# Performance work log

Measured on AMD Instinct MI355X. Metric: run time of the kernel, lower is better.

Reference implementation:

```python
import jax, jax.numpy as jnp
import numpy as np

B, N, R = 16, 512, 10
DE, DR, DOUT = 256, 64, 256

def setup_inputs() -> dict:
    key = jax.random.key(0)
    k1, k2, k3, k4 = jax.random.split(key, 4)
    node_features = jax.random.normal(k1, (B, N, DE), dtype=jnp.float32)
    relation_features = jax.random.normal(k2, (B, R, DR), dtype=jnp.float32)
    adj = jax.random.uniform(k3, (B, R, N, N), dtype=jnp.float32)
    in_dim = (DE + DR) * R
    bound = float(np.sqrt(6.0 / (in_dim + DOUT)))  # xavier_uniform
    W = jax.random.uniform(k4, (DOUT, in_dim), dtype=jnp.float32, minval=-bound, maxval=bound)
    bias = jnp.zeros((DOUT,), dtype=jnp.float32)
    return {"node_features": node_features, "relation_features": relation_features,
            "adj": adj, "W": W, "bias": bias}

def reference(node_features, relation_features, adj, W, bias):
    # adj: [B,R,N,N]; node_features: [B,N,De]; relation_features: [B,R,Dr]
    # Per relation r: bmm(adj[:,r], cat([node, rel_r broadcast], -1))
    # Node part: adj @ node_features for every relation at once.
    node_part = jnp.einsum('brnm,bmd->brnd', adj, node_features)      # [B,R,N,De]
    # Relation part: adj @ (rel_r repeated over rows) == rowsum(adj) * rel_r
    rel_part = adj.sum(axis=-1)[..., None] * relation_features[:, :, None, :]  # [B,R,N,Dr]
    supports = jnp.concatenate([node_part, rel_part], axis=-1)        # [B,R,N,De+Dr]
    supports = supports.transpose(0, 2, 1, 3).reshape(node_features.shape[0],
                                                      node_features.shape[1], -1)  # [B,N,R*(De+Dr)]
    return supports @ W.T + bias
```

## Files before the change

kernel.cpp:

```cpp
#include <hip/hip_runtime.h>
#include <stdint.h>

#define B_     16
#define N_     512
#define R_     10
#define DE_    256
#define DR_    64
#define DOUT_  256
#define INDIM_ 3200
#define BLK_   320
#define RN_    5120
#define SPLITS_ 5

typedef __bf16          v8bf  __attribute__((ext_vector_type(8)));
typedef unsigned short  v8us  __attribute__((ext_vector_type(8)));
typedef float           f32x4 __attribute__((ext_vector_type(4)));

static __device__ __forceinline__ unsigned short f2b(float f) {
  union { float f; unsigned u; } c; c.f = f;
  unsigned r = c.u + 0x7FFFu + ((c.u >> 16) & 1u);
  return (unsigned short)(r >> 16);
}

static __device__ __forceinline__ v8bf us2bf(v8us u) {
  union { v8us u; v8bf b; } c; c.u = u; return c.b;
}

static __device__ __forceinline__ void gl_lds16(const void* g, void* l) {
  __builtin_amdgcn_global_load_lds(
      (const __attribute__((address_space(1))) void*)g,
      (__attribute__((address_space(3))) void*)l, 16, 0, 0);
}

__global__ void prep_nodeB(const float* __restrict__ nf, unsigned short* __restrict__ nodeB) {
  const size_t base = (size_t)blockIdx.x * 8192;
  const int tid = threadIdx.x;
#pragma unroll
  for (int p = 0; p < 4; ++p) {
    size_t off = base + (size_t)p * 2048 + (size_t)tid * 8;
    float4 x = *(const float4*)(nf + off);
    float4 y = *(const float4*)(nf + off + 4);
    v8us u;
    u[0] = f2b(x.x); u[1] = f2b(x.y); u[2] = f2b(x.z); u[3] = f2b(x.w);
    u[4] = f2b(y.x); u[5] = f2b(y.y); u[6] = f2b(y.z); u[7] = f2b(y.w);
    *(v8us*)(nodeB + off) = u;
  }
}

__global__ void prep_W(const float* __restrict__ W, unsigned short* __restrict__ Wn) {
  int idx = blockIdx.x * 256 + threadIdx.x;
  int r = idx >> 16;
  int o = (idx >> 8) & 255;
  int d = idx & 255;
  Wn[idx] = f2b(W[(size_t)o * INDIM_ + r * BLK_ + d]);
}

__global__ void prep_U(const float* __restrict__ rel, const float* __restrict__ W,
                       float* __restrict__ Uf) {
  int idx = blockIdx.x * 256 + threadIdx.x;
  int o  = idx & 255;
  int br = idx >> 8;
  int r  = br % R_;
  const float* rp = rel + (size_t)br * DR_;
  const float* wp = W + (size_t)o * INDIM_ + r * BLK_ + DE_;
  float v = 0.f;
#pragma unroll 8
  for (int d = 0; d < DR_; ++d) v += rp[d] * wp[d];
  Uf[idx] = v;
}

__global__ void stageA_gemm(const unsigned short* __restrict__ nodeB,
                            const unsigned short* __restrict__ WnB,
                            const float* __restrict__ Uf,
                            unsigned short* __restrict__ Gp) {
  __shared__ unsigned short Al[128 * 64];
  __shared__ unsigned short Bl[128 * 64];
  const int br = blockIdx.x;
  const int b  = br / R_, r = br % R_;
  const int o0 = blockIdx.y * 128;
  const int m0 = blockIdx.z * 128;
  const int tid  = threadIdx.x;
  const int lane = tid & 63;
  const int wave = tid >> 6;
  const int wm = wave >> 1, wn = wave & 1;
  const int quad = lane >> 4, l16 = lane & 15;

  const unsigned short* Wb = WnB + (size_t)r * (DOUT_ * DE_);
  const unsigned short* Nb = nodeB + (size_t)b * (N_ * DE_);

  f32x4 acc[4][4];
#pragma unroll
  for (int i = 0; i < 4; ++i)
#pragma unroll
    for (int j = 0; j < 4; ++j) acc[i][j] = f32x4{0.f, 0.f, 0.f, 0.f};

  for (int dk = 0; dk < DE_; dk += 64) {
#pragma unroll
    for (int it = 0; it < 4; ++it) {
      int rowblk = it * 32 + wave * 8;
      int rl = rowblk + (lane >> 3);
      int kc = (lane & 7) ^ (rl & 7);
      gl_lds16(Wb + (size_t)(o0 + rl) * DE_ + dk + kc * 8, Al + rowblk * 64);
      gl_lds16(Nb + (size_t)(m0 + rl) * DE_ + dk + kc * 8, Bl + rowblk * 64);
    }
    __syncthreads();
#pragma unroll
    for (int ks = 0; ks < 2; ++ks) {
      const int kb = ks * 4;
      v8bf av[4], bv[4];
#pragma unroll
      for (int mi = 0; mi < 4; ++mi) {
        int m = wm * 64 + mi * 16 + l16;
        av[mi] = us2bf(*(const v8us*)(Al + m * 64 + (((kb + quad) ^ (m & 7)) * 8)));
      }
#pragma unroll
      for (int ni = 0; ni < 4; ++ni) {
        int c = wn * 64 + ni * 16 + l16;
        bv[ni] = us2bf(*(const v8us*)(Bl + c * 64 + (((kb + quad) ^ (c & 7)) * 8)));
      }
#pragma unroll
      for (int mi = 0; mi < 4; ++mi)
#pragma unroll
        for (int ni = 0; ni < 4; ++ni)
          acc[mi][ni] = __builtin_amdgcn_mfma_f32_16x16x32_bf16(av[mi], bv[ni], acc[mi][ni], 0, 0, 0);
    }
    __syncthreads();
  }

#pragma unroll
  for (int mi = 0; mi < 4; ++mi)
#pragma unroll
    for (int t = 0; t < 4; ++t) {
      int o = o0 + wm * 64 + mi * 16 + quad * 4 + t;
      float u = Uf[(size_t)br * DOUT_ + o];
      unsigned short* grow = Gp + ((size_t)(b * DOUT_ + o)) * RN_ + r * N_ + m0;
#pragma unroll
      for (int ni = 0; ni < 4; ++ni) {
        int m = wn * 64 + ni * 16 + l16;
        grow[m] = f2b(acc[mi][ni][t] + u);
      }
    }
}

__global__ __launch_bounds__(256, 3)
void stageB_gemm(const float* __restrict__ adj,
                 const unsigned short* __restrict__ Gp,
                 float* __restrict__ part) {
  __shared__ unsigned short Al[64 * 64];
  __shared__ unsigned short Bl[256 * 64];
  const int b  = blockIdx.x;
  const int n0 = blockIdx.y * 64;
  const int sp = blockIdx.z;
  const int tid  = threadIdx.x;
  const int lane = tid & 63;
  const int wave = tid >> 6;
  const int quad = lane >> 4, l16 = lane & 15;

  const float* Ab = adj + (size_t)b * (R_ * N_ * N_);
  const unsigned short* Gb = Gp + (size_t)b * (DOUT_ * RN_);

  f32x4 acc[4][4];
#pragma unroll
  for (int i = 0; i < 4; ++i)
#pragma unroll
    for (int j = 0; j < 4; ++j) acc[i][j] = f32x4{0.f, 0.f, 0.f, 0.f};

  const int arow = tid >> 2;
  const int acb  = tid & 3;
  const float* arp = Ab + (size_t)(n0 + arow) * N_ + acb * 16;

  float4 p0, p1, p2, p3;
  {
    const float* g = arp + (size_t)(sp * 2) * (N_ * N_);
    p0 = *(const float4*)(g);
    p1 = *(const float4*)(g + 4);
    p2 = *(const float4*)(g + 8);
    p3 = *(const float4*)(g + 12);
  }

  for (int it = 0; it < 16; ++it) {
    const int r  = sp * 2 + (it >> 3);
    const int k0 = r * N_ + (it & 7) * 64;
#pragma unroll
    for (int s = 0; s < 8; ++s) {
      int rowblk = s * 32 + wave * 8;
      int rl = rowblk + (lane >> 3);
      int kc = (lane & 7) ^ (rl & 7);
      gl_lds16(Gb + (size_t)rl * RN_ + k0 + kc * 8, Bl + rowblk * 64);
    }
    {
      v8us u0, u1;
      u0[0] = f2b(p0.x); u0[1] = f2b(p0.y); u0[2] = f2b(p0.z); u0[3] = f2b(p0.w);
      u0[4] = f2b(p1.x); u0[5] = f2b(p1.y); u0[6] = f2b(p1.z); u0[7] = f2b(p1.w);
      u1[0] = f2b(p2.x); u1[1] = f2b(p2.y); u1[2] = f2b(p2.z); u1[3] = f2b(p2.w);
      u1[4] = f2b(p3.x); u1[5] = f2b(p3.y); u1[6] = f2b(p3.z); u1[7] = f2b(p3.w);
      int c0 = (acb * 2)     ^ (arow & 7);
      int c1 = (acb * 2 + 1) ^ (arow & 7);
      *(v8us*)(Al + arow * 64 + c0 * 8) = u0;
      *(v8us*)(Al + arow * 64 + c1 * 8) = u1;
    }
    if (it < 15) {
      const int rn = sp * 2 + ((it + 1) >> 3);
      const float* g = arp + (size_t)rn * (N_ * N_) + ((it + 1) & 7) * 64;
      p0 = *(const float4*)(g);
      p1 = *(const float4*)(g + 4);
      p2 = *(const float4*)(g + 8);
      p3 = *(const float4*)(g + 12);
    }
    __syncthreads();
#pragma unroll
    for (int ks = 0; ks < 2; ++ks) {
      const int kb = ks * 4;
      v8bf av[4], bv[4];
#pragma unroll
      for (int mi = 0; mi < 4; ++mi) {
        int m = mi * 16 + l16;
        av[mi] = us2bf(*(const v8us*)(Al + m * 64 + (((kb + quad) ^ (m & 7)) * 8)));
      }
#pragma unroll
      for (int ni = 0; ni < 4; ++ni) {
        int o = wave * 64 + ni * 16 + l16;
        bv[ni] = us2bf(*(const v8us*)(Bl + o * 64 + (((kb + quad) ^ (o & 7)) * 8)));
      }
#pragma unroll
      for (int mi = 0; mi < 4; ++mi)
#pragma unroll
        for (int ni = 0; ni < 4; ++ni)
          acc[mi][ni] = __builtin_amdgcn_mfma_f32_16x16x32_bf16(av[mi], bv[ni], acc[mi][ni], 0, 0, 0);
    }
    __syncthreads();
  }

  float* pb = part + (((size_t)sp * B_ + b) * N_) * DOUT_;
#pragma unroll
  for (int mi = 0; mi < 4; ++mi)
#pragma unroll
    for (int t = 0; t < 4; ++t) {
      int row = n0 + mi * 16 + quad * 4 + t;
#pragma unroll
      for (int ni = 0; ni < 4; ++ni) {
        int col = wave * 64 + ni * 16 + l16;
        pb[(size_t)row * DOUT_ + col] = acc[mi][ni][t];
      }
    }
}

__global__ void reduce_out(const float* __restrict__ part, const float* __restrict__ bias,
                           float* __restrict__ out) {
  const size_t idx = (size_t)blockIdx.x * 256 + threadIdx.x;
  const size_t stride = (size_t)B_ * N_ * DOUT_ / 4;
  f32x4 a = *(const f32x4*)(bias + (idx & 63) * 4);
#pragma unroll
  for (int s = 0; s < SPLITS_; ++s) {
    f32x4 p = *(const f32x4*)((const float*)part + (stride * s + idx) * 4);
    a += p;
  }
  *(f32x4*)(out + idx * 4) = a;
}

extern "C" void kernel_launch(void* const* d_in, const int* in_sizes, int n_in,
                              void* d_out, int out_size, void* d_ws, size_t ws_size,
                              hipStream_t stream) {
  const float* node = (const float*)d_in[0];
  const float* rel  = (const float*)d_in[1];
  const float* adj  = (const float*)d_in[2];
  const float* W    = (const float*)d_in[3];
  const float* bias = (const float*)d_in[4];
  float* out = (float*)d_out;

  char* ws = (char*)d_ws;
  unsigned short* nodeB = (unsigned short*)(ws);
  unsigned short* WnB   = (unsigned short*)(ws + ((size_t)5 << 20));
  float*          Uf    = (float*)         (ws + ((size_t)7 << 20));
  unsigned short* Gp    = (unsigned short*)(ws + ((size_t)8 << 20));
  float*          part  = (float*)         (ws + ((size_t)48 << 20));

  prep_nodeB<<<dim3((B_ * N_ * DE_) / 8192), 256, 0, stream>>>(node, nodeB);
  prep_W<<<dim3((R_ * DOUT_ * DE_) / 256), 256, 0, stream>>>(W, WnB);
  prep_U<<<dim3((B_ * R_ * DOUT_) / 256), 256, 0, stream>>>(rel, W, Uf);
  stageA_gemm<<<dim3(B_ * R_, DOUT_ / 128, N_ / 128), 256, 0, stream>>>(nodeB, WnB, Uf, Gp);
  stageB_gemm<<<dim3(B_, N_ / 64, SPLITS_), 256, 0, stream>>>(adj, Gp, part);
  reduce_out<<<dim3((B_ * N_ * DOUT_ / 4) / 256), 256, 0, stream>>>(part, bias, out);
}
```

Before: 321.9 us.

## Merge prep kernels, stage Gp stores through LDS, shrink stageB row tile

The three preprocessing kernels become a single launch that branches on block index, and the W conversion is vectorized to four elements per thread. stageA now writes its bf16 output tile into shared memory and then stores it to Gp with coalesced 16-byte writes, replacing scattered 2-byte stores. stageB halves its row tile from 64 to 32, which doubles the grid and raises launch_bounds occupancy to 4 blocks per CU. The smaller tile means each block re-reads the full 256-column Gp tile for half as many rows, doubling Gp traffic from L2 in exchange for more parallelism.

Measured after the change: 314.9 us. -2.2%, faster.

```diff
diff --git a/kernel.cpp b/kernel.cpp
--- a/kernel.cpp
+++ b/kernel.cpp
@@ -14,6 +14,7 @@
 
 typedef __bf16          v8bf  __attribute__((ext_vector_type(8)));
 typedef unsigned short  v8us  __attribute__((ext_vector_type(8)));
+typedef unsigned short  v4us  __attribute__((ext_vector_type(4)));
 typedef float           f32x4 __attribute__((ext_vector_type(4)));
 
 static __device__ __forceinline__ unsigned short f2b(float f) {
@@ -32,49 +33,55 @@
       (__attribute__((address_space(3))) void*)l, 16, 0, 0);
 }
 
-__global__ void prep_nodeB(const float* __restrict__ nf, unsigned short* __restrict__ nodeB) {
-  const size_t base = (size_t)blockIdx.x * 8192;
+__global__ void prep_all(const float* __restrict__ nf, const float* __restrict__ W,
+                         const float* __restrict__ rel,
+                         unsigned short* __restrict__ nodeB,
+                         unsigned short* __restrict__ WnB,
+                         float* __restrict__ Uf) {
+  const int bb = blockIdx.x;
   const int tid = threadIdx.x;
-#pragma unroll
-  for (int p = 0; p < 4; ++p) {
-    size_t off = base + (size_t)p * 2048 + (size_t)tid * 8;
-    float4 x = *(const float4*)(nf + off);
-    float4 y = *(const float4*)(nf + off + 4);
-    v8us u;
+  if (bb < 256) {
+    const size_t base = (size_t)bb * 8192;
+#pragma unroll
+    for (int p = 0; p < 4; ++p) {
+      size_t off = base + (size_t)p * 2048 + (size_t)tid * 8;
+      float4 x = *(const float4*)(nf + off);
+      float4 y = *(const float4*)(nf + off + 4);
+      v8us u;
+      u[0] = f2b(x.x); u[1] = f2b(x.y); u[2] = f2b(x.z); u[3] = f2b(x.w);
+      u[4] = f2b(y.x); u[5] = f2b(y.y); u[6] = f2b(y.z); u[7] = f2b(y.w);
+      *(v8us*)(nodeB + off) = u;
+    }
+  } else if (bb < 896) {
+    int idx = (bb - 256) * 1024 + tid * 4;
+    int r = idx >> 16;
+    int o = (idx >> 8) & 255;
+    int d = idx & 255;
+    float4 x = *(const float4*)(W + (size_t)o * INDIM_ + r * BLK_ + d);
+    v4us u;
     u[0] = f2b(x.x); u[1] = f2b(x.y); u[2] = f2b(x.z); u[3] = f2b(x.w);
-    u[4] = f2b(y.x); u[5] = f2b(y.y); u[6] = f2b(y.z); u[7] = f2b(y.w);
-    *(v8us*)(nodeB + off) = u;
-  }
-}
-
-__global__ void prep_W(const float* __restrict__ W, unsigned short* __restrict__ Wn) {
-  int idx = blockIdx.x * 256 + threadIdx.x;
-  int r = idx >> 16;
-  int o = (idx >> 8) & 255;
-  int d = idx & 255;
-  Wn[idx] = f2b(W[(size_t)o * INDIM_ + r * BLK_ + d]);
-}
-
-__global__ void prep_U(const float* __restrict__ rel, const float* __restrict__ W,
-                       float* __restrict__ Uf) {
-  int idx = blockIdx.x * 256 + threadIdx.x;
-  int o  = idx & 255;
-  int br = idx >> 8;
-  int r  = br % R_;
-  const float* rp = rel + (size_t)br * DR_;
-  const float* wp = W + (size_t)o * INDIM_ + r * BLK_ + DE_;
-  float v = 0.f;
+    *(v4us*)(WnB + idx) = u;
+  } else {
+    int idx = (bb - 896) * 256 + tid;
+    int o  = idx & 255;
+    int br = idx >> 8;
+    int r  = br % R_;
+    const float* rp = rel + (size_t)br * DR_;
+    const float* wp = W + (size_t)o * INDIM_ + r * BLK_ + DE_;
+    float v = 0.f;
 #pragma unroll 8
-  for (int d = 0; d < DR_; ++d) v += rp[d] * wp[d];
-  Uf[idx] = v;
+    for (int d = 0; d < DR_; ++d) v += rp[d] * wp[d];
+    Uf[idx] = v;
+  }
 }
 
 __global__ void stageA_gemm(const unsigned short* __restrict__ nodeB,
                             const unsigned short* __restrict__ WnB,
                             const float* __restrict__ Uf,
                             unsigned short* __restrict__ Gp) {
-  __shared__ unsigned short Al[128 * 64];
-  __shared__ unsigned short Bl[128 * 64];
+  __shared__ unsigned short S[128 * 128];
+  unsigned short* Al = S;
+  unsigned short* Bl = S + 128 * 64;
   const int br = blockIdx.x;
   const int b  = br / R_, r = br % R_;
   const int o0 = blockIdx.y * 128;
@@ -131,25 +138,33 @@
   for (int mi = 0; mi < 4; ++mi)
 #pragma unroll
     for (int t = 0; t < 4; ++t) {
-      int o = o0 + wm * 64 + mi * 16 + quad * 4 + t;
-      float u = Uf[(size_t)br * DOUT_ + o];
-      unsigned short* grow = Gp + ((size_t)(b * DOUT_ + o)) * RN_ + r * N_ + m0;
-#pragma unroll
-      for (int ni = 0; ni < 4; ++ni) {
-        int m = wn * 64 + ni * 16 + l16;
-        grow[m] = f2b(acc[mi][ni][t] + u);
-      }
-    }
-}
-
-__global__ __launch_bounds__(256, 3)
+      int o_loc = wm * 64 + mi * 16 + quad * 4 + t;
+      float u = Uf[(size_t)br * DOUT_ + o0 + o_loc];
+#pragma unroll
+      for (int ni = 0; ni < 4; ++ni) {
+        int m_loc = wn * 64 + ni * 16 + l16;
+        S[o_loc * 128 + m_loc] = f2b(acc[mi][ni][t] + u);
+      }
+    }
+  __syncthreads();
+#pragma unroll
+  for (int p = 0; p < 8; ++p) {
+    int idx16 = p * 2048 + tid * 8;
+    int orow = idx16 >> 7;
+    int moff = idx16 & 127;
+    unsigned short* dst = Gp + ((size_t)(b * DOUT_ + o0 + orow)) * RN_ + r * N_ + m0 + moff;
+    *(v8us*)dst = *(const v8us*)(S + idx16);
+  }
+}
+
+__global__ __launch_bounds__(256, 4)
 void stageB_gemm(const float* __restrict__ adj,
                  const unsigned short* __restrict__ Gp,
                  float* __restrict__ part) {
-  __shared__ unsigned short Al[64 * 64];
+  __shared__ unsigned short Al[32 * 64];
   __shared__ unsigned short Bl[256 * 64];
   const int b  = blockIdx.x;
-  const int n0 = blockIdx.y * 64;
+  const int n0 = blockIdx.y * 32;
   const int sp = blockIdx.z;
   const int tid  = threadIdx.x;
   const int lane = tid & 63;
@@ -159,23 +174,21 @@
   const float* Ab = adj + (size_t)b * (R_ * N_ * N_);
   const unsigned short* Gb = Gp + (size_t)b * (DOUT_ * RN_);
 
-  f32x4 acc[4][4];
-#pragma unroll
-  for (int i = 0; i < 4; ++i)
+  f32x4 acc[2][4];
+#pragma unroll
+  for (int i = 0; i < 2; ++i)
 #pragma unroll
     for (int j = 0; j < 4; ++j) acc[i][j] = f32x4{0.f, 0.f, 0.f, 0.f};
 
-  const int arow = tid >> 2;
-  const int acb  = tid & 3;
-  const float* arp = Ab + (size_t)(n0 + arow) * N_ + acb * 16;
-
-  float4 p0, p1, p2, p3;
+  const int arow = tid >> 3;
+  const int ac8  = tid & 7;
+  const float* arp = Ab + (size_t)(n0 + arow) * N_ + ac8 * 8;
+
+  float4 p0, p1;
   {
     const float* g = arp + (size_t)(sp * 2) * (N_ * N_);
     p0 = *(const float4*)(g);
     p1 = *(const float4*)(g + 4);
-    p2 = *(const float4*)(g + 8);
-    p3 = *(const float4*)(g + 12);
   }
 
   for (int it = 0; it < 16; ++it) {
@@ -189,31 +202,25 @@
       gl_lds16(Gb + (size_t)rl * RN_ + k0 + kc * 8, Bl + rowblk * 64);
     }
     {
-      v8us u0, u1;
-      u0[0] = f2b(p0.x); u0[1] = f2b(p0.y); u0[2] = f2b(p0.z); u0[3] = f2b(p0.w);
-      u0[4] = f2b(p1.x); u0[5] = f2b(p1.y); u0[6] = f2b(p1.z); u0[7] = f2b(p1.w);
-      u1[0] = f2b(p2.x); u1[1] = f2b(p2.y); u1[2] = f2b(p2.z); u1[3] = f2b(p2.w);
-      u1[4] = f2b(p3.x); u1[5] = f2b(p3.y); u1[6] = f2b(p3.z); u1[7] = f2b(p3.w);
-      int c0 = (acb * 2)     ^ (arow & 7);
-      int c1 = (acb * 2 + 1) ^ (arow & 7);
-      *(v8us*)(Al + arow * 64 + c0 * 8) = u0;
-      *(v8us*)(Al + arow * 64 + c1 * 8) = u1;
+      v8us u;
+      u[0] = f2b(p0.x); u[1] = f2b(p0.y); u[2] = f2b(p0.z); u[3] = f2b(p0.w);
+      u[4] = f2b(p1.x); u[5] = f2b(p1.y); u[6] = f2b(p1.z); u[7] = f2b(p1.w);
+      int cs = ac8 ^ (arow & 7);
+      *(v8us*)(Al + arow * 64 + cs * 8) = u;
     }
     if (it < 15) {
       const int rn = sp * 2 + ((it + 1) >> 3);
       const float* g = arp + (size_t)rn * (N_ * N_) + ((it + 1) & 7) * 64;
       p0 = *(const float4*)(g);
       p1 = *(const float4*)(g + 4);
-      p2 = *(const float4*)(g + 8);
-      p3 = *(const float4*)(g + 12);
     }
     __syncthreads();
 #pragma unroll
     for (int ks = 0; ks < 2; ++ks) {
       const int kb = ks * 4;
-      v8bf av[4], bv[4];
-#pragma unroll
-      for (int mi = 0; mi < 4; ++mi) {
+      v8bf av[2], bv[4];
+#pragma unroll
+      for (int mi = 0; mi < 2; ++mi) {
         int m = mi * 16 + l16;
         av[mi] = us2bf(*(const v8us*)(Al + m * 64 + (((kb + quad) ^ (m & 7)) * 8)));
       }
@@ -223,7 +230,7 @@
         bv[ni] = us2bf(*(const v8us*)(Bl + o * 64 + (((kb + quad) ^ (o & 7)) * 8)));
       }
 #pragma unroll
-      for (int mi = 0; mi < 4; ++mi)
+      for (int mi = 0; mi < 2; ++mi)
 #pragma unroll
         for (int ni = 0; ni < 4; ++ni)
           acc[mi][ni] = __builtin_amdgcn_mfma_f32_16x16x32_bf16(av[mi], bv[ni], acc[mi][ni], 0, 0, 0);
@@ -233,7 +240,7 @@
 
   float* pb = part + (((size_t)sp * B_ + b) * N_) * DOUT_;
 #pragma unroll
-  for (int mi = 0; mi < 4; ++mi)
+  for (int mi = 0; mi < 2; ++mi)
 #pragma unroll
     for (int t = 0; t < 4; ++t) {
       int row = n0 + mi * 16 + quad * 4 + t;
@@ -275,10 +282,8 @@
   unsigned short* Gp    = (unsigned short*)(ws + ((size_t)8 << 20));
   float*          part  = (float*)         (ws + ((size_t)48 << 20));
 
-  prep_nodeB<<<dim3((B_ * N_ * DE_) / 8192), 256, 0, stream>>>(node, nodeB);
-  prep_W<<<dim3((R_ * DOUT_ * DE_) / 256), 256, 0, stream>>>(W, WnB);
-  prep_U<<<dim3((B_ * R_ * DOUT_) / 256), 256, 0, stream>>>(rel, W, Uf);
+  prep_all<<<dim3(1056), 256, 0, stream>>>(node, W, rel, nodeB, WnB, Uf);
   stageA_gemm<<<dim3(B_ * R_, DOUT_ / 128, N_ / 128), 256, 0, stream>>>(nodeB, WnB, Uf, Gp);
-  stageB_gemm<<<dim3(B_, N_ / 64, SPLITS_), 256, 0, stream>>>(adj, Gp, part);
+  stageB_gemm<<<dim3(B_, N_ / 32, SPLITS_), 256, 0, stream>>>(adj, Gp, part);
   reduce_out<<<dim3((B_ * N_ * DOUT_ / 4) / 256), 256, 0, stream>>>(part, bias, out);
 }
```
